# Kernel tuning notes

Hardware: AMD Instinct MI355X
Metric: run time of the kernel (lower is better)

Reference implementation:

```python
import jax, jax.numpy as jnp
import numpy as np

D_MODEL = 2048
N_HEAD = 32
N_KV_HEAD = 8
N_REP = N_HEAD // N_KV_HEAD
D_K = D_MODEL // N_HEAD
THETA = 10000.0
B, S = 2, 1024


def setup_inputs() -> dict:
    key = jax.random.key(0)
    ks = jax.random.split(key, 9)
    sd = 1.0 / np.sqrt(D_MODEL)
    return {
        "x": jax.random.normal(ks[0], (B, S, D_MODEL), jnp.float32),
        "Wq": jax.random.normal(ks[1], (D_MODEL, D_MODEL), jnp.float32) * sd,
        "bq": jax.random.normal(ks[2], (D_MODEL,), jnp.float32) * 0.02,
        "Wk": jax.random.normal(ks[3], (D_MODEL, N_KV_HEAD * D_K), jnp.float32) * sd,
        "bk": jax.random.normal(ks[4], (N_KV_HEAD * D_K,), jnp.float32) * 0.02,
        "Wv": jax.random.normal(ks[5], (D_MODEL, N_KV_HEAD * D_K), jnp.float32) * sd,
        "bv": jax.random.normal(ks[6], (N_KV_HEAD * D_K,), jnp.float32) * 0.02,
        "Wo": jax.random.normal(ks[7], (D_MODEL, D_MODEL), jnp.float32) * sd,
        "bo": jax.random.normal(ks[8], (D_MODEL,), jnp.float32) * 0.02,
    }


def _apply_rope(t, pos):
    # t: [b, h, s, d_k], pos: [s]
    half = D_K // 2
    inv_freq = 1.0 / (THETA ** (jnp.arange(half, dtype=jnp.float32) * 2.0 / D_K))
    ang = pos[:, None].astype(jnp.float32) * inv_freq[None, :]  # [s, half]
    cos = jnp.cos(ang)[None, None]  # [1,1,s,half]
    sin = jnp.sin(ang)[None, None]
    te = t[..., 0::2]
    to = t[..., 1::2]
    re = te * cos - to * sin
    ro = te * sin + to * cos
    return jnp.stack([re, ro], axis=-1).reshape(t.shape)


def reference(x, Wq, bq, Wk, bk, Wv, bv, Wo, bo):
    b, s, _ = x.shape
    q = (x @ Wq + bq).reshape(b, s, N_HEAD, D_K).transpose(0, 2, 1, 3)
    k = (x @ Wk + bk).reshape(b, s, N_KV_HEAD, D_K).transpose(0, 2, 1, 3)
    v = (x @ Wv + bv).reshape(b, s, N_KV_HEAD, D_K).transpose(0, 2, 1, 3)
    pos = jnp.arange(s)
    q = _apply_rope(q, pos)
    k = _apply_rope(k, pos)
    # GQA head repeat: [b, n_kv, s, d] -> [b, n_head, s, d]
    k = jnp.repeat(k, N_REP, axis=1)
    v = jnp.repeat(v, N_REP, axis=1)
    scores = jnp.einsum('bhnd,bhmd->bhnm', q, k) / jnp.sqrt(jnp.float32(D_K))
    mask = jnp.tril(jnp.ones((s, s), dtype=bool))
    scores = jnp.where(mask[None, None], scores, jnp.float32(-jnp.inf))
    probs = jax.nn.softmax(scores, axis=-1)
    out = jnp.einsum('bhnm,bhmd->bhnd', probs, v)
    out = out.transpose(0, 2, 1, 3).reshape(b, s, D_MODEL)
    return out @ Wo + bo
```

## Files before the change

### kernel.cpp

```cpp
#include <hip/hip_runtime.h>
#include <hip/hip_bf16.h>

#define D_MODEL 2048
#define N_HEAD 32
#define N_KV_HEAD 8
#define N_REP 4
#define D_K 64
#define S_LEN 1024
#define B_SZ 2
#define M_ROWS (B_SZ * S_LEN)
#define KV_DIM (N_KV_HEAD * D_K)
#define QKV_N 3072
#define KOFF 2048
#define VOFF 2560
#define LOG2E 1.44269504088896f
#define TAB_N (S_LEN * 32)

typedef __attribute__((ext_vector_type(8))) short short8;
typedef __attribute__((ext_vector_type(4))) float f32x4;
typedef __attribute__((ext_vector_type(16))) float f32x16;

#define EXP2F(x) __builtin_amdgcn_exp2f(x)

__device__ inline unsigned short f2bf(float f) {
    union { float f; unsigned int u; } x{f};
    unsigned int r = x.u + 0x7fffu + ((x.u >> 16) & 1u);
    return (unsigned short)(r >> 16);
}
__device__ inline float bf2f(unsigned short b) {
    union { unsigned int u; float f; } x; x.u = ((unsigned int)b) << 16; return x.f;
}
__device__ inline void store_c(float* p, float v) { *p = v; }
__device__ inline void store_c(unsigned short* p, float v) { *p = f2bf(v); }

__device__ inline void load_lds16(const unsigned short* g, unsigned short* l) {
    __builtin_amdgcn_global_load_lds(
        (const __attribute__((address_space(1))) unsigned int*)g,
        (__attribute__((address_space(3))) unsigned int*)l, 16, 0, 0);
}

__device__ __forceinline__ unsigned int permpack(float hi_f, float lo_f) {
    union { float f; unsigned int u; } a{hi_f}, b{lo_f};
    return __builtin_amdgcn_perm(a.u, b.u, 0x07060302u);
}

__global__ __launch_bounds__(256) void wprep_kernel(
        const float* __restrict__ Wq_, const float* __restrict__ Wk_,
        const float* __restrict__ Wv_, const float* __restrict__ Wo_,
        unsigned short* __restrict__ WtQKV, unsigned short* __restrict__ WtO) {
    const float* src; unsigned short* dst; int N;
    switch (blockIdx.z) {
        case 0: src = Wq_; dst = WtQKV; N = D_MODEL; break;
        case 1: src = Wk_; dst = WtQKV + (size_t)KOFF * D_MODEL; N = KV_DIM; break;
        case 2: src = Wv_; dst = WtQKV + (size_t)VOFF * D_MODEL; N = KV_DIM; break;
        default: src = Wo_; dst = WtO; N = D_MODEL; break;
    }
    int n0 = blockIdx.x * 64;
    if (n0 >= N) return;
    int k0 = blockIdx.y * 64;
    int t = threadIdx.x;
    int n = n0 + (t >> 2);
    int ks = k0 + (t & 3) * 16;
    unsigned int pk[8];
#pragma unroll
    for (int i = 0; i < 8; i++) {
        float a = src[(size_t)(ks + 2 * i) * N + n];
        float b = src[(size_t)(ks + 2 * i + 1) * N + n];
        pk[i] = (unsigned int)f2bf(a) | ((unsigned int)f2bf(b) << 16);
    }
    uint4* d = (uint4*)&dst[(size_t)n * D_MODEL + ks];
    d[0] = make_uint4(pk[0], pk[1], pk[2], pk[3]);
    d[1] = make_uint4(pk[4], pk[5], pk[6], pk[7]);
}

__global__ void cast_bf_kernel(const float* __restrict__ src,
                               unsigned short* __restrict__ dst, int n4) {
    int idx = blockIdx.x * blockDim.x + threadIdx.x;
    if (idx >= n4) return;
    float4 v = ((const float4*)src)[idx];
    unsigned int lo = (unsigned int)f2bf(v.x) | ((unsigned int)f2bf(v.y) << 16);
    unsigned int hi = (unsigned int)f2bf(v.z) | ((unsigned int)f2bf(v.w) << 16);
    ((uint2*)dst)[idx] = make_uint2(lo, hi);
}

__global__ void prep_small_kernel(const float* __restrict__ bq, const float* __restrict__ bk,
                                  const float* __restrict__ bv, float* __restrict__ dst,
                                  float2* __restrict__ tab) {
    int i = blockIdx.x * blockDim.x + threadIdx.x;
    if (i < QKV_N) {
        dst[i] = (i < KOFF) ? bq[i] : (i < VOFF) ? bk[i - KOFF] : bv[i - VOFF];
    }
    int j = i - QKV_N;
    if (j >= 0 && j < TAB_N) {
        int s = j >> 5, p = j & 31;
        float invf = EXP2F((float)p * -0.41524101186f);
        float ang = (float)s * invf;
        tab[j] = make_float2(__cosf(ang), __sinf(ang));
    }
}

template <typename TC, bool ROPE>
__global__ __launch_bounds__(256) void gemm_bf16_kernel(
        const unsigned short* __restrict__ A,
        const unsigned short* __restrict__ Bt,
        const float* __restrict__ bias,
        const float2* __restrict__ rtab,
        TC* __restrict__ C, int M, int N, int K) {
    __shared__ unsigned short As[128 * 64];
    __shared__ unsigned short Bs[64 * 64];
    const int tid = threadIdx.x, lane = tid & 63;
    const int w = tid >> 6, wm = w >> 1, wn = w & 1;
    const int quad = lane >> 4, lr = lane & 15;
    const int bm = blockIdx.y * 128, bn = blockIdx.x * 64;

    f32x4 acc[4][2];
#pragma unroll
    for (int i = 0; i < 4; i++)
#pragma unroll
        for (int j = 0; j < 2; j++) acc[i][j] = (f32x4){0.f, 0.f, 0.f, 0.f};

    for (int k0 = 0; k0 < K; k0 += 64) {
        __syncthreads();
#pragma unroll
        for (int it = 0; it < 4; it++) {
            int slot = it * 256 + tid;
            int row = slot >> 3;
            int qc = (slot & 7) ^ (row & 7);
            load_lds16(A + (size_t)(bm + row) * K + k0 + qc * 8, &As[slot * 8]);
        }
#pragma unroll
        for (int it = 0; it < 2; it++) {
            int slot = it * 256 + tid;
            int row = slot >> 3;
            int qc = (slot & 7) ^ (row & 7);
            load_lds16(Bt + (size_t)(bn + row) * K + k0 + qc * 8, &Bs[slot * 8]);
        }
        __syncthreads();
#pragma unroll
        for (int ks = 0; ks < 2; ks++) {
            short8 af[4], bf[2];
#pragma unroll
            for (int i = 0; i < 4; i++) {
                int row = wm * 64 + i * 16 + lr;
                af[i] = *(const short8*)&As[(row * 8 + ((ks * 4 + quad) ^ (lr & 7))) * 8];
            }
#pragma unroll
            for (int j = 0; j < 2; j++) {
                int row = wn * 32 + j * 16 + lr;
                bf[j] = *(const short8*)&Bs[(row * 8 + ((ks * 4 + quad) ^ (lr & 7))) * 8];
            }
#pragma unroll
            for (int i = 0; i < 4; i++)
#pragma unroll
                for (int j = 0; j < 2; j++)
                    acc[i][j] = __builtin_amdgcn_mfma_f32_16x16x32_bf16(af[i], bf[j], acc[i][j], 0, 0, 0);
        }
    }
#pragma unroll
    for (int i = 0; i < 4; i++) {
#pragma unroll
        for (int j = 0; j < 2; j++) {
            int col = bn + wn * 32 + j * 16 + lr;
            int row0 = bm + wm * 64 + i * 16 + quad * 4;
            float bj = bias[col];
            if constexpr (ROPE) {
                bool isv = col >= VOFF;
                bool isq = col < KOFF;
                int ip = (col & 63) >> 1;
                bool even = !(lr & 1);
#pragma unroll
                for (int r = 0; r < 4; r++) {
                    float v = acc[i][j][r] + bj;
                    float pv = __shfl_xor(v, 1);
                    float outv = v;
                    if (!isv) {
                        int s = (row0 + r) & (S_LEN - 1);
                        float2 cs = rtab[s * 32 + ip];
                        outv = v * cs.x + (even ? -pv : pv) * cs.y;
                        if (isq) outv *= 0.125f * LOG2E;
                    }
                    store_c(&C[(size_t)(row0 + r) * N + col], outv);
                }
            } else {
#pragma unroll
                for (int r = 0; r < 4; r++)
                    store_c(&C[(size_t)(row0 + r) * N + col], acc[i][j][r] + bj);
            }
        }
    }
}

#define AST 72
struct Pre { uint4 k0, k1, v0, v1; };

__device__ __forceinline__ void issue_pre(const unsigned short* kb,
                                          const unsigned short* vb,
                                          int j0, int tid, Pre& p) {
    int f0 = tid, f1 = tid + 256;
    p.k0 = *(const uint4*)(kb + (size_t)(j0 + (f0 >> 3)) * QKV_N + (f0 & 7) * 8);
    p.k1 = *(const uint4*)(kb + (size_t)(j0 + (f1 >> 3)) * QKV_N + (f1 & 7) * 8);
    int kp = tid & 31, dg = tid >> 5;
    p.v0 = *(const uint4*)(vb + (size_t)(j0 + 2 * kp) * QKV_N + dg * 8);
    p.v1 = *(const uint4*)(vb + (size_t)(j0 + 2 * kp + 1) * QKV_N + dg * 8);
}
__device__ __forceinline__ void commit_pre(unsigned short* Ks, unsigned short* Vt,
                                           int tid, const Pre& p) {
    int f0 = tid, f1 = tid + 256;
    *(uint4*)&Ks[(f0 >> 3) * AST + (f0 & 7) * 8] = p.k0;
    *(uint4*)&Ks[(f1 >> 3) * AST + (f1 & 7) * 8] = p.k1;
    int kp = tid & 31, dg = tid >> 5;
    const unsigned short* ta = (const unsigned short*)&p.v0;
    const unsigned short* tb = (const unsigned short*)&p.v1;
#pragma unroll
    for (int i = 0; i < 8; i++) {
        unsigned int pk = (unsigned int)ta[i] | ((unsigned int)tb[i] << 16);
        *(unsigned int*)&Vt[(dg * 8 + i) * AST + 2 * kp] = pk;
    }
}

__global__ __launch_bounds__(256) void attn_mfma_kernel(
        const unsigned short* __restrict__ qkv,
        unsigned short* __restrict__ obf) {
    __shared__ unsigned short SM[2 * 64 * AST];
    unsigned short* Ks = SM;
    unsigned short* Vt = SM + 64 * AST;
    const int tid = threadIdx.x;
    const int w = tid >> 6, lane = tid & 63;
    const int lq = lane & 31, hi = lane >> 5;
    const int hi8 = hi * 8, hi4 = hi * 4;
    const int h = blockIdx.y, b = blockIdx.z;
    const int kvh = h >> 2;
    const unsigned short* kb = qkv + (size_t)(b * S_LEN) * QKV_N + KOFF + kvh * D_K;
    const unsigned short* vb = qkv + (size_t)(b * S_LEN) * QKV_N + VOFF + kvh * D_K;

    const int qt = b ? 7 - (int)blockIdx.x : (int)blockIdx.x;
    const int nt = 2 * qt + 2;
    const int qw0 = qt * 128 + w * 32;
    const int qg = qw0 + lq;

    short8 aq[4];
    {
        const unsigned short* qp = qkv + (size_t)(b * S_LEN + qg) * QKV_N + h * D_K + hi8;
#pragma unroll
        for (int st = 0; st < 4; st++) aq[st] = *(const short8*)(qp + st * 16);
    }
    f32x16 oacc[2];
#pragma unroll
    for (int dt = 0; dt < 2; dt++)
#pragma unroll
        for (int r = 0; r < 16; r++) oacc[dt][r] = 0.f;
    float m = -1e30f, l = 0.f;

    Pre pre;
    issue_pre(kb, vb, 0, tid, pre);
    for (int t = 0; t < nt; t++) {
        __syncthreads();
        commit_pre(Ks, Vt, tid, pre);
        __syncthreads();
        if (t + 1 < nt) issue_pre(kb, vb, (t + 1) * 64, tid, pre);
        const int t64 = t * 64;
        if (t64 > qw0 + 31) continue;

        f32x16 s0, s1;
#pragma unroll
        for (int r = 0; r < 16; r++) { s0[r] = 0.f; s1[r] = 0.f; }
#pragma unroll
        for (int st = 0; st < 4; st++) {
            short8 k0 = *(const short8*)&Ks[lq * AST + st * 16 + hi8];
            short8 k1 = *(const short8*)&Ks[(32 + lq) * AST + st * 16 + hi8];
            s0 = __builtin_amdgcn_mfma_f32_32x32x16_bf16(k0, aq[st], s0, 0, 0, 0);
            s1 = __builtin_amdgcn_mfma_f32_32x32x16_bf16(k1, aq[st], s1, 0, 0, 0);
        }
        float px[32];
#pragma unroll
        for (int r = 0; r < 16; r++) { px[r] = s0[r]; px[16 + r] = s1[r]; }
        if (t64 + 63 > qw0) {
#pragma unroll
            for (int kh = 0; kh < 2; kh++)
#pragma unroll
                for (int r = 0; r < 16; r++) {
                    int kg = t64 + kh * 32 + ((r & 3) + 8 * (r >> 2)) + hi4;
                    if (kg > qg) px[kh * 16 + r] = -1e30f;
                }
        }
        float tm[16];
#pragma unroll
        for (int i = 0; i < 16; i++) tm[i] = fmaxf(px[i], px[i + 16]);
#pragma unroll
        for (int i = 0; i < 8; i++) tm[i] = fmaxf(tm[i], tm[i + 8]);
#pragma unroll
        for (int i = 0; i < 4; i++) tm[i] = fmaxf(tm[i], tm[i + 4]);
        float lmax = fmaxf(fmaxf(tm[0], tm[1]), fmaxf(tm[2], tm[3]));
        union { float f; unsigned int u; } mb{lmax};
        auto rr = __builtin_amdgcn_permlane32_swap((int)mb.u, (int)mb.u, false, false);
        union { unsigned int u; float f; } ra, rb;
        ra.u = (unsigned int)rr[0];
        rb.u = (unsigned int)rr[1];
        float mn = fmaxf(m, fmaxf(ra.f, rb.f));
        float corr = EXP2F(m - mn);
        m = mn;
        float p[32], pm[32];
#pragma unroll
        for (int i = 0; i < 32; i++) {
            p[i] = EXP2F(px[i] - mn);
            union { float f; unsigned int u; } pu{p[i]};
            pu.u &= 0xFFFF0000u;
            pm[i] = pu.f;
        }
        float ts[16];
#pragma unroll
        for (int i = 0; i < 16; i++) ts[i] = pm[i] + pm[i + 16];
#pragma unroll
        for (int i = 0; i < 8; i++) ts[i] = ts[i] + ts[i + 8];
#pragma unroll
        for (int i = 0; i < 4; i++) ts[i] = ts[i] + ts[i + 4];
        float lsum = (ts[0] + ts[1]) + (ts[2] + ts[3]);
        union { float f; unsigned int u; } sb{lsum};
        auto rr2 = __builtin_amdgcn_permlane32_swap((int)sb.u, (int)sb.u, false, false);
        union { unsigned int u; float f; } sa2, sb2;
        sa2.u = (unsigned int)rr2[0];
        sb2.u = (unsigned int)rr2[1];
        l = l * corr + (sa2.f + sb2.f);
#pragma unroll
        for (int dt = 0; dt < 2; dt++)
#pragma unroll
            for (int r = 0; r < 16; r++) oacc[dt][r] *= corr;
        short8 pf[4];
#pragma unroll
        for (int kh = 0; kh < 2; kh++)
#pragma unroll
            for (int s = 0; s < 2; s++) {
                int base = kh * 16 + 8 * s;
                unsigned int a01 = permpack(p[base + 1], p[base + 0]);
                unsigned int a23 = permpack(p[base + 3], p[base + 2]);
                unsigned int a45 = permpack(p[base + 5], p[base + 4]);
                unsigned int a67 = permpack(p[base + 7], p[base + 6]);
                auto r02 = __builtin_amdgcn_permlane32_swap((int)a01, (int)a45, false, false);
                auto r13 = __builtin_amdgcn_permlane32_swap((int)a23, (int)a67, false, false);
                union { unsigned int wd[4]; short8 v; } pk;
                pk.wd[0] = (unsigned int)r02[0];
                pk.wd[1] = (unsigned int)r13[0];
                pk.wd[2] = (unsigned int)r02[1];
                pk.wd[3] = (unsigned int)r13[1];
                pf[kh * 2 + s] = pk.v;
            }
#pragma unroll
        for (int dt = 0; dt < 2; dt++)
#pragma unroll
            for (int sl = 0; sl < 4; sl++) {
                short8 va = *(const short8*)&Vt[(dt * 32 + lq) * AST + sl * 16 + hi8];
                oacc[dt] = __builtin_amdgcn_mfma_f32_32x32x16_bf16(va, pf[sl], oacc[dt], 0, 0, 0);
            }
    }
    __syncthreads();
    float inv = 1.f / l;
    unsigned short* Os = SM + w * 32 * AST;
#pragma unroll
    for (int dt = 0; dt < 2; dt++)
#pragma unroll
        for (int j = 0; j < 8; j++) {
            int d = dt * 32 + ((2 * j) & 3) + 8 * (j >> 1) + hi4;
            unsigned int pk = (unsigned int)f2bf(oacc[dt][2 * j] * inv)
                            | ((unsigned int)f2bf(oacc[dt][2 * j + 1] * inv) << 16);
            *(unsigned int*)&Os[lq * AST + d] = pk;
        }
    __syncthreads();
#pragma unroll
    for (int j = 0; j < 4; j++) {
        int row = j * 8 + (lane >> 3);
        short8 v = *(const short8*)&Os[row * AST + (lane & 7) * 8];
        int qrow = b * S_LEN + qw0 + row;
        *(short8*)&obf[(size_t)qrow * D_MODEL + h * D_K + (lane & 7) * 8] = v;
    }
}

extern "C" void kernel_launch(void* const* d_in, const int* in_sizes, int n_in,
                              void* d_out, int out_size, void* d_ws, size_t ws_size,
                              hipStream_t stream) {
    const float* x  = (const float*)d_in[0];
    const float* Wq = (const float*)d_in[1];
    const float* bq = (const float*)d_in[2];
    const float* Wk = (const float*)d_in[3];
    const float* bk = (const float*)d_in[4];
    const float* Wv = (const float*)d_in[5];
    const float* bv = (const float*)d_in[6];
    const float* Wo = (const float*)d_in[7];
    const float* bo = (const float*)d_in[8];
    float* out = (float*)d_out;

    unsigned short* xbf   = (unsigned short*)d_ws;
    unsigned short* WtQKV = xbf + (size_t)M_ROWS * D_MODEL;
    unsigned short* WtO   = WtQKV + (size_t)QKV_N * D_MODEL;
    unsigned short* qkv   = WtO + (size_t)D_MODEL * D_MODEL;
    float* bias_qkv       = (float*)(qkv + (size_t)M_ROWS * QKV_N);
    float2* rtab          = (float2*)(bias_qkv + QKV_N);
    unsigned short* obf   = xbf;

    dim3 gb(256);

    cast_bf_kernel<<<(M_ROWS * D_MODEL / 4 + 255) / 256, gb, 0, stream>>>(x, xbf, M_ROWS * D_MODEL / 4);
    wprep_kernel<<<dim3(32, 32, 4), gb, 0, stream>>>(Wq, Wk, Wv, Wo, WtQKV, WtO);
    prep_small_kernel<<<(QKV_N + TAB_N + 255) / 256, gb, 0, stream>>>(bq, bk, bv, bias_qkv, rtab);
    gemm_bf16_kernel<unsigned short, true><<<dim3(QKV_N / 64, M_ROWS / 128), gb, 0, stream>>>(
        xbf, WtQKV, bias_qkv, rtab, qkv, M_ROWS, QKV_N, D_MODEL);
    attn_mfma_kernel<<<dim3(8, N_HEAD, B_SZ), gb, 0, stream>>>(qkv, obf);
    gemm_bf16_kernel<float, false><<<dim3(D_MODEL / 64, M_ROWS / 128), gb, 0, stream>>>(
        obf, WtO, bo, nullptr, out, M_ROWS, D_MODEL, D_MODEL);
}
```

Before: 225.2 us.

## Double-buffer attention K/V tiles, lazily rescale softmax, merge prep kernels

The attention kernel now keeps two K/V tile buffers in LDS, so the next tile is committed while the current one is computed. This drops one of the two barriers per iteration. Online-softmax rescaling of the accumulators is skipped unless the running max grows past a threshold, and MFMA sections get raised wave priority. The x fp32-to-bf16 cast is folded into the weight prep kernel to save a launch. The costs are double the LDS per block, which may lower occupancy, and a lazy-rescale threshold that lets exponent values reach up to 2^8 before rescaling.

```diff
diff --git a/kernel.cpp b/kernel.cpp
--- a/kernel.cpp
+++ b/kernel.cpp
@@ -44,12 +44,27 @@
     return __builtin_amdgcn_perm(a.u, b.u, 0x07060302u);
 }
 
-__global__ __launch_bounds__(256) void wprep_kernel(
+__global__ __launch_bounds__(256) void prep_kernel(
+        const float* __restrict__ x,
         const float* __restrict__ Wq_, const float* __restrict__ Wk_,
         const float* __restrict__ Wv_, const float* __restrict__ Wo_,
+        unsigned short* __restrict__ xbf,
         unsigned short* __restrict__ WtQKV, unsigned short* __restrict__ WtO) {
+    const int z = blockIdx.z;
+    if (z >= 4) {
+        int idx = ((z - 4) * 1024 + blockIdx.y * 32 + blockIdx.x) * 256 + threadIdx.x;
+#pragma unroll
+        for (int half = 0; half < 2; half++) {
+            int i = idx + half * 524288;
+            float4 v = ((const float4*)x)[i];
+            unsigned int lo = (unsigned int)f2bf(v.x) | ((unsigned int)f2bf(v.y) << 16);
+            unsigned int hi = (unsigned int)f2bf(v.z) | ((unsigned int)f2bf(v.w) << 16);
+            ((uint2*)xbf)[i] = make_uint2(lo, hi);
+        }
+        return;
+    }
     const float* src; unsigned short* dst; int N;
-    switch (blockIdx.z) {
+    switch (z) {
         case 0: src = Wq_; dst = WtQKV; N = D_MODEL; break;
         case 1: src = Wk_; dst = WtQKV + (size_t)KOFF * D_MODEL; N = KV_DIM; break;
         case 2: src = Wv_; dst = WtQKV + (size_t)VOFF * D_MODEL; N = KV_DIM; break;
@@ -71,16 +86,6 @@
     uint4* d = (uint4*)&dst[(size_t)n * D_MODEL + ks];
     d[0] = make_uint4(pk[0], pk[1], pk[2], pk[3]);
     d[1] = make_uint4(pk[4], pk[5], pk[6], pk[7]);
-}
-
-__global__ void cast_bf_kernel(const float* __restrict__ src,
-                               unsigned short* __restrict__ dst, int n4) {
-    int idx = blockIdx.x * blockDim.x + threadIdx.x;
-    if (idx >= n4) return;
-    float4 v = ((const float4*)src)[idx];
-    unsigned int lo = (unsigned int)f2bf(v.x) | ((unsigned int)f2bf(v.y) << 16);
-    unsigned int hi = (unsigned int)f2bf(v.z) | ((unsigned int)f2bf(v.w) << 16);
-    ((uint2*)dst)[idx] = make_uint2(lo, hi);
 }
 
 __global__ void prep_small_kernel(const float* __restrict__ bq, const float* __restrict__ bk,
@@ -191,6 +196,7 @@
 }
 
 #define AST 72
+#define RESCALE_THR 8.0f
 struct Pre { uint4 k0, k1, v0, v1; };
 
 __device__ __forceinline__ void issue_pre(const unsigned short* kb,
@@ -221,9 +227,7 @@
 __global__ __launch_bounds__(256) void attn_mfma_kernel(
         const unsigned short* __restrict__ qkv,
         unsigned short* __restrict__ obf) {
-    __shared__ unsigned short SM[2 * 64 * AST];
-    unsigned short* Ks = SM;
-    unsigned short* Vt = SM + 64 * AST;
+    __shared__ unsigned short SM[4 * 64 * AST];
     const int tid = threadIdx.x;
     const int w = tid >> 6, lane = tid & 63;
     const int lq = lane & 31, hi = lane >> 5;
@@ -253,106 +257,121 @@
 
     Pre pre;
     issue_pre(kb, vb, 0, tid, pre);
+    commit_pre(SM, SM + 64 * AST, tid, pre);
+    if (nt > 1) issue_pre(kb, vb, 64, tid, pre);
+    __syncthreads();
+
     for (int t = 0; t < nt; t++) {
+        const int par = t & 1;
+        unsigned short* Ks = SM + par * (2 * 64 * AST);
+        unsigned short* Vt = Ks + 64 * AST;
+        const int t64 = t * 64;
+        if (t64 <= qw0 + 31) {
+            f32x16 s0, s1;
+#pragma unroll
+            for (int r = 0; r < 16; r++) { s0[r] = 0.f; s1[r] = 0.f; }
+            __builtin_amdgcn_s_setprio(1);
+#pragma unroll
+            for (int st = 0; st < 4; st++) {
+                short8 k0 = *(const short8*)&Ks[lq * AST + st * 16 + hi8];
+                short8 k1 = *(const short8*)&Ks[(32 + lq) * AST + st * 16 + hi8];
+                s0 = __builtin_amdgcn_mfma_f32_32x32x16_bf16(k0, aq[st], s0, 0, 0, 0);
+                s1 = __builtin_amdgcn_mfma_f32_32x32x16_bf16(k1, aq[st], s1, 0, 0, 0);
+            }
+            __builtin_amdgcn_s_setprio(0);
+            float px[32];
+#pragma unroll
+            for (int r = 0; r < 16; r++) { px[r] = s0[r]; px[16 + r] = s1[r]; }
+            if (t64 + 63 > qw0) {
+#pragma unroll
+                for (int kh = 0; kh < 2; kh++)
+#pragma unroll
+                    for (int r = 0; r < 16; r++) {
+                        int kg = t64 + kh * 32 + ((r & 3) + 8 * (r >> 2)) + hi4;
+                        if (kg > qg) px[kh * 16 + r] = -1e30f;
+                    }
+            }
+            float tm[16];
+#pragma unroll
+            for (int i = 0; i < 16; i++) tm[i] = fmaxf(px[i], px[i + 16]);
+#pragma unroll
+            for (int i = 0; i < 8; i++) tm[i] = fmaxf(tm[i], tm[i + 8]);
+#pragma unroll
+            for (int i = 0; i < 4; i++) tm[i] = fmaxf(tm[i], tm[i + 4]);
+            float lmax = fmaxf(fmaxf(tm[0], tm[1]), fmaxf(tm[2], tm[3]));
+            union { float f; unsigned int u; } mb{lmax};
+            auto rr = __builtin_amdgcn_permlane32_swap((int)mb.u, (int)mb.u, false, false);
+            union { unsigned int u; float f; } ra, rb;
+            ra.u = (unsigned int)rr[0];
+            rb.u = (unsigned int)rr[1];
+            float mn = fmaxf(m, fmaxf(ra.f, rb.f));
+            if (!__all(mn - m <= RESCALE_THR)) {
+                float corr = EXP2F(m - mn);
+                m = mn;
+                l *= corr;
+#pragma unroll
+                for (int dt = 0; dt < 2; dt++)
+#pragma unroll
+                    for (int r = 0; r < 16; r++) oacc[dt][r] *= corr;
+            }
+            float p[32], pm[32];
+#pragma unroll
+            for (int i = 0; i < 32; i++) {
+                p[i] = EXP2F(px[i] - m);
+                union { float f; unsigned int u; } pu{p[i]};
+                pu.u &= 0xFFFF0000u;
+                pm[i] = pu.f;
+            }
+            float ts[16];
+#pragma unroll
+            for (int i = 0; i < 16; i++) ts[i] = pm[i] + pm[i + 16];
+#pragma unroll
+            for (int i = 0; i < 8; i++) ts[i] = ts[i] + ts[i + 8];
+#pragma unroll
+            for (int i = 0; i < 4; i++) ts[i] = ts[i] + ts[i + 4];
+            float lsum = (ts[0] + ts[1]) + (ts[2] + ts[3]);
+            union { float f; unsigned int u; } sb{lsum};
+            auto rr2 = __builtin_amdgcn_permlane32_swap((int)sb.u, (int)sb.u, false, false);
+            union { unsigned int u; float f; } sa2, sb2;
+            sa2.u = (unsigned int)rr2[0];
+            sb2.u = (unsigned int)rr2[1];
+            l = l + (sa2.f + sb2.f);
+            short8 pf[4];
+#pragma unroll
+            for (int kh = 0; kh < 2; kh++)
+#pragma unroll
+                for (int s = 0; s < 2; s++) {
+                    int base = kh * 16 + 8 * s;
+                    unsigned int a01 = permpack(p[base + 1], p[base + 0]);
+                    unsigned int a23 = permpack(p[base + 3], p[base + 2]);
+                    unsigned int a45 = permpack(p[base + 5], p[base + 4]);
+                    unsigned int a67 = permpack(p[base + 7], p[base + 6]);
+                    auto r02 = __builtin_amdgcn_permlane32_swap((int)a01, (int)a45, false, false);
+                    auto r13 = __builtin_amdgcn_permlane32_swap((int)a23, (int)a67, false, false);
+                    union { unsigned int wd[4]; short8 v; } pk;
+                    pk.wd[0] = (unsigned int)r02[0];
+                    pk.wd[1] = (unsigned int)r13[0];
+                    pk.wd[2] = (unsigned int)r02[1];
+                    pk.wd[3] = (unsigned int)r13[1];
+                    pf[kh * 2 + s] = pk.v;
+                }
+            __builtin_amdgcn_s_setprio(1);
+#pragma unroll
+            for (int dt = 0; dt < 2; dt++)
+#pragma unroll
+                for (int sl = 0; sl < 4; sl++) {
+                    short8 va = *(const short8*)&Vt[(dt * 32 + lq) * AST + sl * 16 + hi8];
+                    oacc[dt] = __builtin_amdgcn_mfma_f32_32x32x16_bf16(va, pf[sl], oacc[dt], 0, 0, 0);
+                }
+            __builtin_amdgcn_s_setprio(0);
+        }
+        if (t + 1 < nt) {
+            unsigned short* Kn = SM + (par ^ 1) * (2 * 64 * AST);
+            commit_pre(Kn, Kn + 64 * AST, tid, pre);
+            if (t + 2 < nt) issue_pre(kb, vb, (t + 2) * 64, tid, pre);
+        }
         __syncthreads();
-        commit_pre(Ks, Vt, tid, pre);
-        __syncthreads();
-        if (t + 1 < nt) issue_pre(kb, vb, (t + 1) * 64, tid, pre);
-        const int t64 = t * 64;
-        if (t64 > qw0 + 31) continue;
-
-        f32x16 s0, s1;
-#pragma unroll
-        for (int r = 0; r < 16; r++) { s0[r] = 0.f; s1[r] = 0.f; }
-#pragma unroll
-        for (int st = 0; st < 4; st++) {
-            short8 k0 = *(const short8*)&Ks[lq * AST + st * 16 + hi8];
-            short8 k1 = *(const short8*)&Ks[(32 + lq) * AST + st * 16 + hi8];
-            s0 = __builtin_amdgcn_mfma_f32_32x32x16_bf16(k0, aq[st], s0, 0, 0, 0);
-            s1 = __builtin_amdgcn_mfma_f32_32x32x16_bf16(k1, aq[st], s1, 0, 0, 0);
-        }
-        float px[32];
-#pragma unroll
-        for (int r = 0; r < 16; r++) { px[r] = s0[r]; px[16 + r] = s1[r]; }
-        if (t64 + 63 > qw0) {
-#pragma unroll
-            for (int kh = 0; kh < 2; kh++)
-#pragma unroll
-                for (int r = 0; r < 16; r++) {
-                    int kg = t64 + kh * 32 + ((r & 3) + 8 * (r >> 2)) + hi4;
-                    if (kg > qg) px[kh * 16 + r] = -1e30f;
-                }
-        }
-        float tm[16];
-#pragma unroll
-        for (int i = 0; i < 16; i++) tm[i] = fmaxf(px[i], px[i + 16]);
-#pragma unroll
-        for (int i = 0; i < 8; i++) tm[i] = fmaxf(tm[i], tm[i + 8]);
-#pragma unroll
-        for (int i = 0; i < 4; i++) tm[i] = fmaxf(tm[i], tm[i + 4]);
-        float lmax = fmaxf(fmaxf(tm[0], tm[1]), fmaxf(tm[2], tm[3]));
-        union { float f; unsigned int u; } mb{lmax};
-        auto rr = __builtin_amdgcn_permlane32_swap((int)mb.u, (int)mb.u, false, false);
-        union { unsigned int u; float f; } ra, rb;
-        ra.u = (unsigned int)rr[0];
-        rb.u = (unsigned int)rr[1];
-        float mn = fmaxf(m, fmaxf(ra.f, rb.f));
-        float corr = EXP2F(m - mn);
-        m = mn;
-        float p[32], pm[32];
-#pragma unroll
-        for (int i = 0; i < 32; i++) {
-            p[i] = EXP2F(px[i] - mn);
-            union { float f; unsigned int u; } pu{p[i]};
-            pu.u &= 0xFFFF0000u;
-            pm[i] = pu.f;
-        }
-        float ts[16];
-#pragma unroll
-        for (int i = 0; i < 16; i++) ts[i] = pm[i] + pm[i + 16];
-#pragma unroll
-        for (int i = 0; i < 8; i++) ts[i] = ts[i] + ts[i + 8];
-#pragma unroll
-        for (int i = 0; i < 4; i++) ts[i] = ts[i] + ts[i + 4];
-        float lsum = (ts[0] + ts[1]) + (ts[2] + ts[3]);
-        union { float f; unsigned int u; } sb{lsum};
-        auto rr2 = __builtin_amdgcn_permlane32_swap((int)sb.u, (int)sb.u, false, false);
-        union { unsigned int u; float f; } sa2, sb2;
-        sa2.u = (unsigned int)rr2[0];
-        sb2.u = (unsigned int)rr2[1];
-        l = l * corr + (sa2.f + sb2.f);
-#pragma unroll
-        for (int dt = 0; dt < 2; dt++)
-#pragma unroll
-            for (int r = 0; r < 16; r++) oacc[dt][r] *= corr;
-        short8 pf[4];
-#pragma unroll
-        for (int kh = 0; kh < 2; kh++)
-#pragma unroll
-            for (int s = 0; s < 2; s++) {
-                int base = kh * 16 + 8 * s;
-                unsigned int a01 = permpack(p[base + 1], p[base + 0]);
-                unsigned int a23 = permpack(p[base + 3], p[base + 2]);
-                unsigned int a45 = permpack(p[base + 5], p[base + 4]);
-                unsigned int a67 = permpack(p[base + 7], p[base + 6]);
-                auto r02 = __builtin_amdgcn_permlane32_swap((int)a01, (int)a45, false, false);
-                auto r13 = __builtin_amdgcn_permlane32_swap((int)a23, (int)a67, false, false);
-                union { unsigned int wd[4]; short8 v; } pk;
-                pk.wd[0] = (unsigned int)r02[0];
-                pk.wd[1] = (unsigned int)r13[0];
-                pk.wd[2] = (unsigned int)r02[1];
-                pk.wd[3] = (unsigned int)r13[1];
-                pf[kh * 2 + s] = pk.v;
-            }
-#pragma unroll
-        for (int dt = 0; dt < 2; dt++)
-#pragma unroll
-            for (int sl = 0; sl < 4; sl++) {
-                short8 va = *(const short8*)&Vt[(dt * 32 + lq) * AST + sl * 16 + hi8];
-                oacc[dt] = __builtin_amdgcn_mfma_f32_32x32x16_bf16(va, pf[sl], oacc[dt], 0, 0, 0);
-            }
-    }
-    __syncthreads();
+    }
     float inv = 1.f / l;
     unsigned short* Os = SM + w * 32 * AST;
 #pragma unroll
@@ -398,8 +417,7 @@
 
     dim3 gb(256);
 
-    cast_bf_kernel<<<(M_ROWS * D_MODEL / 4 + 255) / 256, gb, 0, stream>>>(x, xbf, M_ROWS * D_MODEL / 4);
-    wprep_kernel<<<dim3(32, 32, 4), gb, 0, stream>>>(Wq, Wk, Wv, Wo, WtQKV, WtO);
+    prep_kernel<<<dim3(32, 32, 6), gb, 0, stream>>>(x, Wq, Wk, Wv, Wo, xbf, WtQKV, WtO);
     prep_small_kernel<<<(QKV_N + TAB_N + 255) / 256, gb, 0, stream>>>(bq, bk, bv, bias_qkv, rtab);
     gemm_bf16_kernel<unsigned short, true><<<dim3(QKV_N / 64, M_ROWS / 128), gb, 0, stream>>>(
         xbf, WtQKV, bias_qkv, rtab, qkv, M_ROWS, QKV_N, D_MODEL);
```

After: 218.9 us. 2.8% less time.
